# Kernel tuning notes

Measured on AMD Instinct MI355X. Metric: run time of the kernel, lower is better.

## Reference

```python
import jax, jax.numpy as jnp
import numpy as np

COMMITMENT_COST = 0.25
NUM_EMBEDDINGS = 1024
EMBEDDING_DIM = 256


def setup_inputs() -> dict:
    key = jax.random.key(0)
    k1, k2 = jax.random.split(key)
    inputs = jax.random.normal(k1, (32, 32, 32, EMBEDDING_DIM), dtype=jnp.float32)
    # GlorotUniform-ish init for the [D, K] codebook
    limit = float(np.sqrt(6.0 / (EMBEDDING_DIM + NUM_EMBEDDINGS)))
    w = jax.random.uniform(k2, (EMBEDDING_DIM, NUM_EMBEDDINGS), dtype=jnp.float32,
                           minval=-limit, maxval=limit)
    return {"inputs": inputs, "w": w}


def reference(inputs, w):
    D, K = w.shape
    flat = inputs.reshape(-1, D)                                   # [N, D]
    distances = (jnp.sum(flat * flat, axis=1, keepdims=True)
                 - 2.0 * (flat @ w)
                 + jnp.sum(w * w, axis=0, keepdims=True))          # [N, K]
    enc_idx_flat = jnp.argmin(distances, axis=1)                   # [N]
    encodings = jax.nn.one_hot(enc_idx_flat, K, dtype=inputs.dtype)  # [N, K]
    encoding_indices = enc_idx_flat.reshape(inputs.shape[:-1])     # [B, H, W]
    quantized = jnp.take(w.T, encoding_indices, axis=0)            # [B, H, W, D]

    e_latent_loss = jnp.mean((jax.lax.stop_gradient(quantized) - inputs) ** 2)
    q_latent_loss = jnp.mean((quantized - jax.lax.stop_gradient(inputs)) ** 2)
    loss = q_latent_loss + COMMITMENT_COST * e_latent_loss

    quantized_skip = inputs + jax.lax.stop_gradient(quantized - inputs)

    avg_probs = jnp.mean(encodings, axis=0)                        # [K]
    perplexity = jnp.exp(-jnp.sum(avg_probs * jnp.log(avg_probs + 1e-10)))
    return (quantized_skip, loss, perplexity, encodings, encoding_indices)
```

## Files before the change

### kernel.cpp

```cpp
#include <hip/hip_runtime.h>
#include <cfloat>
#include <cmath>
#include <stdint.h>

#define NROWS 32768
#define DIM   256
#define KC    1024

typedef short bf16x8 __attribute__((ext_vector_type(8)));
typedef float f32x4  __attribute__((ext_vector_type(4)));
typedef float f32x2  __attribute__((ext_vector_type(2)));

__device__ inline unsigned short f2bf(float f) {
    unsigned u = __float_as_uint(f);
    u = (u + 0x7fffu + ((u >> 16) & 1u)) >> 16;
    return (unsigned short)u;
}

__global__ __launch_bounds__(256) void prep_w(const float* __restrict__ w,
                                              uint4* __restrict__ wph,
                                              float* __restrict__ wT) {
    const int t = blockIdx.x * 256 + threadIdx.x;
    const int l = t & 63;
    const int ks = (t >> 6) & 7;
    const int ctg = t >> 9;
    const int c = ctg * 16 + (l & 15);
    const int kbase = ks * 32 + ((l >> 4) << 3);
    union { unsigned short u[8]; uint4 v; } H;
#pragma unroll
    for (int j = 0; j < 8; ++j) {
        float v = w[(size_t)(kbase + j) * KC + c];
        H.u[j] = f2bf(v);
        wT[(size_t)c * DIM + kbase + j] = v;
    }
    wph[t] = H.v;
}

__global__ __launch_bounds__(256) void wnorm_kernel(const float* __restrict__ wT,
                                                    double* __restrict__ wnorm64,
                                                    float* __restrict__ wnormf) {
    const int k = blockIdx.x * 256 + threadIdx.x;
    const float* p = wT + (size_t)k * DIM;
    double acc = 0.0;
#pragma unroll 8
    for (int d = 0; d < DIM; ++d) acc += (double)p[d] * (double)p[d];
    wnorm64[k] = acc;
    wnormf[k] = (float)acc;
}

__global__ __launch_bounds__(256, 4) void vq_screen(
    const float* __restrict__ x,
    const char* __restrict__ wph,
    const float* __restrict__ wnormf,
    int* __restrict__ cand)
{
    const int t = threadIdx.x;
    const int l = t & 63;
    const int wv = t >> 6;
    const int p = blockIdx.x & 1;
    const int rt = blockIdx.x >> 1;
    const int r0 = rt * 64 + wv * 16;
    const char* wp = wph + (size_t)p * 262144;

    bf16x8 ah[8];
    {
        const float* xb = x + (size_t)(r0 + (l & 15)) * DIM + ((l >> 4) << 3);
#pragma unroll
        for (int ks = 0; ks < 8; ++ks) {
            float4 p0 = *(const float4*)(xb + ks * 32);
            float4 p1 = *(const float4*)(xb + ks * 32 + 4);
            float f[8] = {p0.x, p0.y, p0.z, p0.w, p1.x, p1.y, p1.z, p1.w};
            union { unsigned short u[8]; bf16x8 v; } H;
#pragma unroll
            for (int j = 0; j < 8; ++j) H.u[j] = f2bf(f[j]);
            ah[ks] = H.v;
        }
    }

    float tv0[4], tv1[4], tv2[4];
    int   tk0[4], tk1[4], tk2[4];
#pragma unroll
    for (int r = 0; r < 4; ++r) { tv0[r] = tv1[r] = tv2[r] = FLT_MAX; tk0[r] = tk1[r] = tk2[r] = 0; }

#pragma unroll 2
    for (int ctg = 0; ctg < 32; ++ctg) {
        const char* bp = wp + (size_t)ctg * 8192 + l * 16;
        bf16x8 b[8];
#pragma unroll
        for (int ks = 0; ks < 8; ++ks)
            b[ks] = *(const bf16x8*)(bp + ks * 1024);

        f32x4 acc = (f32x4){0.f, 0.f, 0.f, 0.f};
#pragma unroll
        for (int ks = 0; ks < 8; ++ks)
            acc = __builtin_amdgcn_mfma_f32_16x16x32_bf16(ah[ks], b[ks], acc, 0, 0, 0);

        const int k = (p * 32 + ctg) * 16 + (l & 15);
        const float wn = wnormf[k];
#pragma unroll
        for (int r = 0; r < 4; ++r) {
            float sc = fmaf(-2.0f, acc[r], wn);
            if (sc < tv2[r]) {
                if (sc < tv1[r]) {
                    tv2[r] = tv1[r]; tk2[r] = tk1[r];
                    if (sc < tv0[r]) { tv1[r] = tv0[r]; tk1[r] = tk0[r]; tv0[r] = sc; tk0[r] = k; }
                    else             { tv1[r] = sc;     tk1[r] = k; }
                } else { tv2[r] = sc; tk2[r] = k; }
            }
        }
    }

    const float margin = 0.125f;
    const int grpShift = (l >> 4) * 16;
    const unsigned laneMask = (1u << (l & 15)) - 1u;
#pragma unroll
    for (int r = 0; r < 4; ++r) {
        float v = tv0[r];
#pragma unroll
        for (int m = 1; m <= 8; m <<= 1) v = fminf(v, __shfl_xor(v, m));
        const float thr = v + margin;
        const int row = r0 + ((l >> 4) << 2) + r;
        int* creg = cand + ((size_t)row * 2 + p) * 16;
        int base = 0;
        {
            bool c = tv0[r] <= thr;
            unsigned long long bal = __ballot(c);
            unsigned grp = (unsigned)(bal >> grpShift) & 0xFFFFu;
            int pos = base + __popc(grp & laneMask);
            if (c && pos < 7) { creg[1 + pos] = tk0[r]; creg[8 + pos] = __float_as_int(tv0[r]); }
            base += __popc(grp);
        }
        {
            bool c = tv1[r] <= thr;
            unsigned long long bal = __ballot(c);
            unsigned grp = (unsigned)(bal >> grpShift) & 0xFFFFu;
            int pos = base + __popc(grp & laneMask);
            if (c && pos < 7) { creg[1 + pos] = tk1[r]; creg[8 + pos] = __float_as_int(tv1[r]); }
            base += __popc(grp);
        }
        {
            bool c = tv2[r] <= thr;
            unsigned long long bal = __ballot(c);
            unsigned grp = (unsigned)(bal >> grpShift) & 0xFFFFu;
            int pos = base + __popc(grp & laneMask);
            if (c && pos < 7) { creg[1 + pos] = tk2[r]; creg[8 + pos] = __float_as_int(tv2[r]); }
            base += __popc(grp);
        }
        if ((l & 15) == 0) creg[0] = base < 7 ? base : 7;
    }
}

__global__ __launch_bounds__(256) void vq_final(
    const float* __restrict__ x, const float* __restrict__ wT,
    const double* __restrict__ wnorm64,
    const int* __restrict__ cand,
    float* __restrict__ out_q, float* __restrict__ out_idx, float* __restrict__ out_enc,
    int* __restrict__ counts, double* __restrict__ loss_sum)
{
    const int t = threadIdx.x;
    const int l = t & 63;
    const int wv = t >> 6;
    __shared__ double wsum[4];
    const float margin = 0.125f;

    double ls0 = 0.0, ls1 = 0.0, ls2 = 0.0, ls3 = 0.0;
    const int stride = gridDim.x * 4;
    for (int row = blockIdx.x * 4 + wv; row < NROWS; row += stride) {
        const float4 xv = ((const float4*)(x + (size_t)row * DIM))[l];
        const int* c0 = cand + (size_t)row * 32;

        float m = FLT_MAX;
#pragma unroll
        for (int p2 = 0; p2 < 2; ++p2) {
            const int* cp = c0 + p2 * 16;
            const int n = cp[0];
            for (int c = 0; c < n; ++c) m = fminf(m, __int_as_float(cp[8 + c]));
        }
        const float thr = m + margin;

        int bk = 0x7FFFFFFF, cnt = 0;
#pragma unroll
        for (int p2 = 0; p2 < 2; ++p2) {
            const int* cp = c0 + p2 * 16;
            const int n = cp[0];
            for (int c = 0; c < n; ++c)
                if (__int_as_float(cp[8 + c]) <= thr) { ++cnt; bk = cp[1 + c]; }
        }
        if (cnt > 1) {
            double best = 1e300; bk = 0x7FFFFFFF;
#pragma unroll
            for (int p2 = 0; p2 < 2; ++p2) {
                const int* cp = c0 + p2 * 16;
                const int n = cp[0];
                for (int c = 0; c < n; ++c) {
                    if (__int_as_float(cp[8 + c]) > thr) continue;
                    const int k2 = cp[1 + c];
                    const float4 w4 = ((const float4*)(wT + (size_t)k2 * DIM))[l];
                    double d = (double)xv.x * (double)w4.x;
                    d = fma((double)xv.y, (double)w4.y, d);
                    d = fma((double)xv.z, (double)w4.z, d);
                    d = fma((double)xv.w, (double)w4.w, d);
#pragma unroll
                    for (int mm = 32; mm > 0; mm >>= 1) d += __shfl_xor(d, mm);
                    const double s64 = wnorm64[k2] - 2.0 * d;
                    if (s64 < best || (s64 == best && k2 < bk)) { best = s64; bk = k2; }
                }
            }
        }
        const int k = __builtin_amdgcn_readfirstlane(bk);

        const float4 qv = ((const float4*)(wT + (size_t)k * DIM))[l];
        f32x4 o = {xv.x + (qv.x - xv.x), xv.y + (qv.y - xv.y),
                   xv.z + (qv.z - xv.z), xv.w + (qv.w - xv.w)};
        __builtin_nontemporal_store(o, (f32x4*)(out_q + (size_t)row * DIM) + l);
        double dx = (double)qv.x - (double)xv.x; ls0 = fma(dx, dx, ls0);
        dx = (double)qv.y - (double)xv.y; ls1 = fma(dx, dx, ls1);
        dx = (double)qv.z - (double)xv.z; ls2 = fma(dx, dx, ls2);
        dx = (double)qv.w - (double)xv.w; ls3 = fma(dx, dx, ls3);
        f32x2* er2 = (f32x2*)(out_enc + (size_t)row * KC);
        f32x2 z = {0.f, 0.f};
#pragma unroll
        for (int i = 0; i < 8; ++i)
            __builtin_nontemporal_store(z, er2 + i * 64 + l);
        if (l == ((k >> 1) & 63)) out_enc[(size_t)row * KC + k] = 1.0f;
        if (l == 0) {
            out_idx[row] = (float)k;
            atomicAdd(&counts[k], 1);
        }
    }
    double lsum = (ls0 + ls1) + (ls2 + ls3);
#pragma unroll
    for (int off = 32; off > 0; off >>= 1) lsum += __shfl_down(lsum, off);
    if (l == 0) wsum[wv] = lsum;
    __syncthreads();
    if (t == 0) atomicAdd(loss_sum, wsum[0] + wsum[1] + wsum[2] + wsum[3]);
}

__global__ __launch_bounds__(1024) void final_kernel(const int* __restrict__ counts,
                                                     const double* __restrict__ loss_sum,
                                                     float* __restrict__ out_loss,
                                                     float* __restrict__ out_ppl) {
    const int t = threadIdx.x;
    double p = (double)counts[t] * (1.0 / 32768.0);
    double term = -p * log(p + 1e-10);
#pragma unroll
    for (int off = 32; off > 0; off >>= 1) term += __shfl_down(term, off);
    __shared__ double ws[16];
    if ((t & 63) == 0) ws[t >> 6] = term;
    __syncthreads();
    if (t == 0) {
        double s = 0.0;
        for (int i = 0; i < 16; ++i) s += ws[i];
        *out_ppl = (float)exp(s);
        *out_loss = (float)(1.25 * loss_sum[0] * (1.0 / 8388608.0));
    }
}

extern "C" void kernel_launch(void* const* d_in, const int* in_sizes, int n_in,
                              void* d_out, int out_size, void* d_ws, size_t ws_size,
                              hipStream_t stream) {
    const float* x = (const float*)d_in[0];
    const float* w = (const float*)d_in[1];

    float* out = (float*)d_out;
    float* out_q    = out;
    float* out_loss = out + 8388608;
    float* out_ppl  = out + 8388609;
    float* out_enc  = out + 8388610;
    float* out_idx  = out + 8388610 + 33554432;

    char* wsb = (char*)d_ws;
    double* loss_sum = (double*)(wsb + 0);
    int*    counts   = (int*)(wsb + 64);
    double* wnorm64  = (double*)(wsb + 4160);
    float*  wnormf   = (float*)(wsb + 12352);
    float*  wT       = (float*)(wsb + 16448);
    uint4*  wph      = (uint4*)(wsb + 1065024);
    int*    cand     = (int*)(wsb + 1589312);

    (void)hipMemsetAsync(d_ws, 0, 4160, stream);

    prep_w<<<128, 256, 0, stream>>>(w, wph, wT);
    wnorm_kernel<<<4, 256, 0, stream>>>(wT, wnorm64, wnormf);
    vq_screen<<<1024, 256, 0, stream>>>(x, (const char*)wph, wnormf, cand);
    vq_final<<<2048, 256, 0, stream>>>(x, wT, wnorm64, cand,
                                       out_q, out_idx, out_enc, counts, loss_sum);
    final_kernel<<<1, 1024, 0, stream>>>(counts, loss_sum, out_loss, out_ppl);
}
```

Before: 142.9 us.

## Split codebook screen four ways and overlap one-hot zeroing with MFMA screening

The bf16 screening kernel now splits the codebook into four partitions instead of two, doubling the grid, and raises the occupancy hint. Each candidate's index is packed into the low 10 mantissa bits of its score, so the top-3 tracking keeps no separate index registers. The zero-fill of the large one-hot encoding output moves from the final kernel into the compute-bound screen loop, so the memory writes overlap MFMA work; the final kernel only writes the single 1.0 per row. The candidate buffer doubles in size, and packing slightly perturbs the screening scores, which the margin is assumed to absorb.

After: 149.5 us. 4.6% more time.

```diff
diff --git a/kernel.cpp b/kernel.cpp
--- a/kernel.cpp
+++ b/kernel.cpp
@@ -6,6 +6,7 @@
 #define NROWS 32768
 #define DIM   256
 #define KC    1024
+#define MARGIN 0.125f
 
 typedef short bf16x8 __attribute__((ext_vector_type(8)));
 typedef float f32x4  __attribute__((ext_vector_type(4)));
@@ -15,6 +16,9 @@
     unsigned u = __float_as_uint(f);
     u = (u + 0x7fffu + ((u >> 16) & 1u)) >> 16;
     return (unsigned short)u;
+}
+__device__ inline float packsk(float s, int k) {
+    return __int_as_float((__float_as_int(s) & ~1023) | k);
 }
 
 __global__ __launch_bounds__(256) void prep_w(const float* __restrict__ w,
@@ -48,19 +52,20 @@
     wnormf[k] = (float)acc;
 }
 
-__global__ __launch_bounds__(256, 4) void vq_screen(
+__global__ __launch_bounds__(256, 6) void vq_screen(
     const float* __restrict__ x,
     const char* __restrict__ wph,
     const float* __restrict__ wnormf,
-    int* __restrict__ cand)
+    int* __restrict__ cand,
+    float* __restrict__ out_enc)
 {
     const int t = threadIdx.x;
     const int l = t & 63;
     const int wv = t >> 6;
-    const int p = blockIdx.x & 1;
-    const int rt = blockIdx.x >> 1;
+    const int p = blockIdx.x & 3;
+    const int rt = blockIdx.x >> 2;
     const int r0 = rt * 64 + wv * 16;
-    const char* wp = wph + (size_t)p * 262144;
+    const char* wp = wph + (size_t)p * 131072;
 
     bf16x8 ah[8];
     {
@@ -78,39 +83,48 @@
     }
 
     float tv0[4], tv1[4], tv2[4];
-    int   tk0[4], tk1[4], tk2[4];
-#pragma unroll
-    for (int r = 0; r < 4; ++r) { tv0[r] = tv1[r] = tv2[r] = FLT_MAX; tk0[r] = tk1[r] = tk2[r] = 0; }
-
-#pragma unroll 2
-    for (int ctg = 0; ctg < 32; ++ctg) {
-        const char* bp = wp + (size_t)ctg * 8192 + l * 16;
-        bf16x8 b[8];
-#pragma unroll
-        for (int ks = 0; ks < 8; ++ks)
-            b[ks] = *(const bf16x8*)(bp + ks * 1024);
+#pragma unroll
+    for (int r = 0; r < 4; ++r) { tv0[r] = tv1[r] = tv2[r] = FLT_MAX; }
+
+    for (int g = 0; g < 16; ++g) {
+        const char* bp = wp + (size_t)g * 8192 + l * 16;
+        bf16x8 ba[4];
+#pragma unroll
+        for (int i = 0; i < 4; ++i) ba[i] = *(const bf16x8*)(bp + i * 1024);
+
+        {
+            const int zrow = r0 + g;
+            f32x2* er2 = (f32x2*)(out_enc + (size_t)zrow * KC + p * 256);
+            f32x2 z = {0.f, 0.f};
+            __builtin_nontemporal_store(z, er2 + l);
+            __builtin_nontemporal_store(z, er2 + 64 + l);
+        }
 
         f32x4 acc = (f32x4){0.f, 0.f, 0.f, 0.f};
 #pragma unroll
-        for (int ks = 0; ks < 8; ++ks)
-            acc = __builtin_amdgcn_mfma_f32_16x16x32_bf16(ah[ks], b[ks], acc, 0, 0, 0);
-
-        const int k = (p * 32 + ctg) * 16 + (l & 15);
+        for (int i = 0; i < 4; ++i)
+            acc = __builtin_amdgcn_mfma_f32_16x16x32_bf16(ah[i], ba[i], acc, 0, 0, 0);
+#pragma unroll
+        for (int i = 0; i < 4; ++i) ba[i] = *(const bf16x8*)(bp + (4 + i) * 1024);
+#pragma unroll
+        for (int i = 0; i < 4; ++i)
+            acc = __builtin_amdgcn_mfma_f32_16x16x32_bf16(ah[4 + i], ba[i], acc, 0, 0, 0);
+
+        const int k = (p * 16 + g) * 16 + (l & 15);
         const float wn = wnormf[k];
 #pragma unroll
         for (int r = 0; r < 4; ++r) {
-            float sc = fmaf(-2.0f, acc[r], wn);
-            if (sc < tv2[r]) {
-                if (sc < tv1[r]) {
-                    tv2[r] = tv1[r]; tk2[r] = tk1[r];
-                    if (sc < tv0[r]) { tv1[r] = tv0[r]; tk1[r] = tk0[r]; tv0[r] = sc; tk0[r] = k; }
-                    else             { tv1[r] = sc;     tk1[r] = k; }
-                } else { tv2[r] = sc; tk2[r] = k; }
+            float sp = packsk(fmaf(-2.0f, acc[r], wn), k);
+            if (sp < tv2[r]) {
+                if (sp < tv1[r]) {
+                    tv2[r] = tv1[r];
+                    if (sp < tv0[r]) { tv1[r] = tv0[r]; tv0[r] = sp; }
+                    else             { tv1[r] = sp; }
+                } else { tv2[r] = sp; }
             }
         }
     }
 
-    const float margin = 0.125f;
     const int grpShift = (l >> 4) * 16;
     const unsigned laneMask = (1u << (l & 15)) - 1u;
 #pragma unroll
@@ -118,32 +132,21 @@
         float v = tv0[r];
 #pragma unroll
         for (int m = 1; m <= 8; m <<= 1) v = fminf(v, __shfl_xor(v, m));
-        const float thr = v + margin;
+        const float thr = v + MARGIN;
         const int row = r0 + ((l >> 4) << 2) + r;
-        int* creg = cand + ((size_t)row * 2 + p) * 16;
+        int* creg = cand + ((size_t)row * 4 + p) * 16;
         int base = 0;
-        {
-            bool c = tv0[r] <= thr;
+#pragma unroll
+        for (int j = 0; j < 3; ++j) {
+            const float tvj = (j == 0) ? tv0[r] : (j == 1) ? tv1[r] : tv2[r];
+            bool c = tvj <= thr;
             unsigned long long bal = __ballot(c);
             unsigned grp = (unsigned)(bal >> grpShift) & 0xFFFFu;
             int pos = base + __popc(grp & laneMask);
-            if (c && pos < 7) { creg[1 + pos] = tk0[r]; creg[8 + pos] = __float_as_int(tv0[r]); }
-            base += __popc(grp);
-        }
-        {
-            bool c = tv1[r] <= thr;
-            unsigned long long bal = __ballot(c);
-            unsigned grp = (unsigned)(bal >> grpShift) & 0xFFFFu;
-            int pos = base + __popc(grp & laneMask);
-            if (c && pos < 7) { creg[1 + pos] = tk1[r]; creg[8 + pos] = __float_as_int(tv1[r]); }
-            base += __popc(grp);
-        }
-        {
-            bool c = tv2[r] <= thr;
-            unsigned long long bal = __ballot(c);
-            unsigned grp = (unsigned)(bal >> grpShift) & 0xFFFFu;
-            int pos = base + __popc(grp & laneMask);
-            if (c && pos < 7) { creg[1 + pos] = tk2[r]; creg[8 + pos] = __float_as_int(tv2[r]); }
+            if (c && pos < 7) {
+                creg[1 + pos] = __float_as_int(tvj) & 1023;
+                creg[8 + pos] = __float_as_int(tvj);
+            }
             base += __popc(grp);
         }
         if ((l & 15) == 0) creg[0] = base < 7 ? base : 7;
@@ -161,27 +164,26 @@
     const int l = t & 63;
     const int wv = t >> 6;
     __shared__ double wsum[4];
-    const float margin = 0.125f;
 
     double ls0 = 0.0, ls1 = 0.0, ls2 = 0.0, ls3 = 0.0;
     const int stride = gridDim.x * 4;
     for (int row = blockIdx.x * 4 + wv; row < NROWS; row += stride) {
         const float4 xv = ((const float4*)(x + (size_t)row * DIM))[l];
-        const int* c0 = cand + (size_t)row * 32;
+        const int* c0 = cand + (size_t)row * 64;
 
         float m = FLT_MAX;
 #pragma unroll
-        for (int p2 = 0; p2 < 2; ++p2) {
-            const int* cp = c0 + p2 * 16;
+        for (int p4 = 0; p4 < 4; ++p4) {
+            const int* cp = c0 + p4 * 16;
             const int n = cp[0];
             for (int c = 0; c < n; ++c) m = fminf(m, __int_as_float(cp[8 + c]));
         }
-        const float thr = m + margin;
+        const float thr = m + MARGIN;
 
         int bk = 0x7FFFFFFF, cnt = 0;
 #pragma unroll
-        for (int p2 = 0; p2 < 2; ++p2) {
-            const int* cp = c0 + p2 * 16;
+        for (int p4 = 0; p4 < 4; ++p4) {
+            const int* cp = c0 + p4 * 16;
             const int n = cp[0];
             for (int c = 0; c < n; ++c)
                 if (__int_as_float(cp[8 + c]) <= thr) { ++cnt; bk = cp[1 + c]; }
@@ -189,8 +191,8 @@
         if (cnt > 1) {
             double best = 1e300; bk = 0x7FFFFFFF;
 #pragma unroll
-            for (int p2 = 0; p2 < 2; ++p2) {
-                const int* cp = c0 + p2 * 16;
+            for (int p4 = 0; p4 < 4; ++p4) {
+                const int* cp = c0 + p4 * 16;
                 const int n = cp[0];
                 for (int c = 0; c < n; ++c) {
                     if (__int_as_float(cp[8 + c]) > thr) continue;
@@ -217,13 +219,8 @@
         dx = (double)qv.y - (double)xv.y; ls1 = fma(dx, dx, ls1);
         dx = (double)qv.z - (double)xv.z; ls2 = fma(dx, dx, ls2);
         dx = (double)qv.w - (double)xv.w; ls3 = fma(dx, dx, ls3);
-        f32x2* er2 = (f32x2*)(out_enc + (size_t)row * KC);
-        f32x2 z = {0.f, 0.f};
-#pragma unroll
-        for (int i = 0; i < 8; ++i)
-            __builtin_nontemporal_store(z, er2 + i * 64 + l);
-        if (l == ((k >> 1) & 63)) out_enc[(size_t)row * KC + k] = 1.0f;
         if (l == 0) {
+            out_enc[(size_t)row * KC + k] = 1.0f;
             out_idx[row] = (float)k;
             atomicAdd(&counts[k], 1);
         }
@@ -282,7 +279,7 @@
 
     prep_w<<<128, 256, 0, stream>>>(w, wph, wT);
     wnorm_kernel<<<4, 256, 0, stream>>>(wT, wnorm64, wnormf);
-    vq_screen<<<1024, 256, 0, stream>>>(x, (const char*)wph, wnormf, cand);
+    vq_screen<<<2048, 256, 0, stream>>>(x, (const char*)wph, wnormf, cand, out_enc);
     vq_final<<<2048, 256, 0, stream>>>(x, wT, wnorm64, cand,
                                        out_q, out_idx, out_enc, counts, loss_sum);
     final_kernel<<<1, 1024, 0, stream>>>(counts, loss_sum, out_loss, out_ppl);
```
